# Performance work log

Hardware: AMD Instinct MI355X
Metric: run time of the kernel (lower is better)

## Reference

```python
import jax, jax.numpy as jnp
import numpy as np

N_HEAD = 16

def setup_inputs() -> dict:
    key = jax.random.key(0)
    k0, k1, k2, k3 = jax.random.split(key, 4)
    S, E, H, T = 2048, 1024, N_HEAD, 4096
    d = E // H
    return {
        "x": jax.random.normal(k0, (S, E), jnp.float32),
        "past": jax.random.normal(k1, (2, H, T, d), jnp.float32),  # stacked [pk, pv]
        "W1": jax.random.normal(k2, (E, 3 * E), jnp.float32) * 0.02,  # c_attn (Conv1D k=1 == linear)
        "b1": jnp.zeros((3 * E,), jnp.float32),
        "W2": jax.random.normal(k3, (E, E), jnp.float32) * 0.02,  # c_proj
        "b2": jnp.zeros((E,), jnp.float32),
        "past_length": 2048,
    }


def reference(x, past, W1, b1, W2, b2, past_length):
    H = N_HEAD
    S, E = x.shape
    d = E // H

    c = x @ W1 + b1  # [S, 3E]
    q, k, v = jnp.split(c, 3, axis=1)

    def split_heads(t):  # [S, E] -> [H, S, d]
        return jnp.transpose(t.reshape(S, H, d), (1, 0, 2))

    q, k, v = split_heads(q), split_heads(k), split_heads(v)

    pk, pv = past[0], past[1]  # [H, T, d]
    k = jax.lax.dynamic_update_slice_in_dim(pk, k, past_length, axis=1)
    v = jax.lax.dynamic_update_slice_in_dim(pv, v, past_length, axis=1)

    # attention scores [H, S, T]
    w = jnp.einsum('hid,hjd->hij', q, k) / np.sqrt(d)
    ns = k.shape[1]
    i = jnp.arange(S)[:, None]
    j = jnp.arange(ns)[None, :]
    b = (i >= j - past_length).astype(w.dtype)
    w = w * b - jnp.float32(1e10) * (1 - b)
    w = jax.nn.softmax(w, axis=-1)

    a = jnp.einsum('hij,hjd->hid', w, v)  # [H, S, d]
    # faithful to original: start index clamps to 0 since axis len == S
    a = jax.lax.dynamic_slice_in_dim(a, past_length, S, axis=1)
    a = jnp.transpose(a, (1, 0, 2)).reshape(S, E)  # merge heads

    out = a @ W2 + b2
    new_cache = jnp.stack([k, v], axis=0)
    return out, new_cache
```

## Files before the change

kernel.cpp:

```cpp
#include <hip/hip_runtime.h>
#include <hip/hip_bf16.h>
#include <stdint.h>


#define S_LEN 2048
#define E_DIM 1024
#define NHEAD 16
#define HDIM  64
#define T_LEN 4096
#define PASTL 2048

typedef __bf16 bf16x8 __attribute__((ext_vector_type(8)));
typedef __bf16 bf16x4 __attribute__((ext_vector_type(4)));
typedef float  f32x4  __attribute__((ext_vector_type(4)));

static __device__ __forceinline__ f32x4 mfma_bf16(bf16x8 a, bf16x8 b, f32x4 c) {
  return __builtin_amdgcn_mfma_f32_16x16x32_bf16(a, b, c, 0, 0, 0);
}

static __device__ __forceinline__ unsigned int f2bf(float f) {
  union { float f; unsigned int u; } v; v.f = f;
  unsigned int u = v.u;
  return (u + 0x7fffu + ((u >> 16) & 1u)) >> 16;
}

static __device__ __forceinline__ float bf2f(unsigned short u) {
  union { unsigned int u; float f; } v; v.u = (unsigned int)u << 16;
  return v.f;
}

#define GLOBAL_LOAD_LDS16(gptr, lptr)                                              \
  __builtin_amdgcn_global_load_lds(                                                \
      (const __attribute__((address_space(1))) unsigned int*)(gptr),               \
      (__attribute__((address_space(3))) unsigned int*)(lptr), 16, 0, 0)

__global__ __launch_bounds__(256) void prep_kernel(
    const float* __restrict__ past, const float* __restrict__ x,
    const float* __restrict__ W1, const float* __restrict__ W2,
    float* __restrict__ cache, unsigned short* __restrict__ kb,
    unsigned short* __restrict__ xb, unsigned short* __restrict__ w1t,
    unsigned short* __restrict__ w2t, unsigned short* __restrict__ vtb) {
  __shared__ float tile[64][65];
  const int bid = blockIdx.x;
  const int tid = threadIdx.x;
  const int tx = tid & 63, ty = tid >> 6;

  if (bid < 512) {
    const int h = bid >> 5;
    const int t0 = (bid & 31) * 64;
    const float* in = past + (size_t)(NHEAD + h) * T_LEN * HDIM;
    unsigned short* outp = vtb + (size_t)h * HDIM * T_LEN;
#pragma unroll
    for (int r = 0; r < 64; r += 4)
      tile[r + ty][tx] = in[(size_t)(t0 + r + ty) * HDIM + tx];
    __syncthreads();
#pragma unroll
    for (int r = 0; r < 64; r += 4)
      outp[(size_t)(r + ty) * T_LEN + t0 + tx] = f2bf(tile[tx][r + ty]);
  } else if (bid < 1536) {
    const float* in;
    unsigned short* outp;
    int rows, cols, c0, r0;
    if (bid < 1280) {
      int u = bid - 512;
      in = W1; outp = w1t; rows = 1024; cols = 3072;
      c0 = (u % 48) * 64; r0 = (u / 48) * 64;
    } else {
      int u = bid - 1280;
      in = W2; outp = w2t; rows = 1024; cols = 1024;
      c0 = (u & 15) * 64; r0 = (u >> 4) * 64;
    }
#pragma unroll
    for (int r = 0; r < 64; r += 4)
      tile[r + ty][tx] = in[(size_t)(r0 + r + ty) * cols + c0 + tx];
    __syncthreads();
#pragma unroll
    for (int r = 0; r < 64; r += 4)
      outp[(size_t)(c0 + r + ty) * rows + r0 + tx] = f2bf(tile[tx][r + ty]);
  } else {
    const int n4p = (2 * NHEAD * PASTL * HDIM) / 4;
    const int n4x = (S_LEN * E_DIM) / 4;
    for (int i = (bid - 1536) * 256 + tid; i < n4p + n4x; i += 2048 * 256) {
      if (i < n4p) {
        int e = i * 4;
        int d = e & 63;
        int t = (e >> 6) & (PASTL - 1);
        int hh = (e >> 17) & (NHEAD - 1);
        int kv = e >> 21;
        size_t full = (((size_t)kv * NHEAD + hh) * T_LEN + t) * HDIM + d;
        float4 v = *(const float4*)(past + full);
        *(float4*)(cache + full) = v;
        if (kv == 0) {
          ushort4 u;
          u.x = f2bf(v.x); u.y = f2bf(v.y); u.z = f2bf(v.z); u.w = f2bf(v.w);
          *(ushort4*)(kb + full) = u;
        }
      } else {
        int j = i - n4p;
        float4 v = ((const float4*)x)[j];
        ushort4 u;
        u.x = f2bf(v.x); u.y = f2bf(v.y); u.z = f2bf(v.z); u.w = f2bf(v.w);
        ((ushort4*)xb)[j] = u;
      }
    }
  }
}

template <int MODE>
__global__ __launch_bounds__(256) void gemm_bt_kernel(
    const unsigned short* __restrict__ A, const unsigned short* __restrict__ Bt,
    const float* __restrict__ bias, int K,
    float* __restrict__ out_f32, unsigned short* __restrict__ qb,
    float* __restrict__ cache_k, float* __restrict__ cache_v,
    unsigned short* __restrict__ kb, unsigned short* __restrict__ vtb) {
  __shared__ alignas(16) unsigned short As[64 * 64];
  __shared__ alignas(16) unsigned short Bs[128 * 64];
  const int NPX = (MODE == 0) ? 3 : 1;
  const int bid = blockIdx.x;
  const int xcd = bid & 7;
  const int loc = bid >> 3;
  const int n_idx = xcd * NPX + loc % NPX;
  const int m_idx = loc / NPX;
  const int m0 = m_idx * 64, n0 = n_idx * 128;

  const int tid = threadIdx.x;
  const int lane = tid & 63;
  const int w = tid >> 6;
  const int wm = w >> 1, wn = w & 1;
  const int lr = lane & 15;
  const int lg = lane >> 4;

  f32x4 acc[2][4];
#pragma unroll
  for (int i = 0; i < 2; ++i)
#pragma unroll
    for (int j = 0; j < 4; ++j) acc[i][j] = f32x4{0.f, 0.f, 0.f, 0.f};

  const int srow = tid >> 3;
  const int sseg = (tid & 7) ^ (srow & 7);
  const unsigned short* ga0 = A + (size_t)(m0 + srow) * K + sseg * 8;
  const unsigned short* gb0 = Bt + (size_t)(n0 + srow) * K + sseg * 8;

  for (int k0 = 0; k0 < K; k0 += 64) {
    GLOBAL_LOAD_LDS16(ga0 + k0, (char*)As + tid * 16);
    GLOBAL_LOAD_LDS16(ga0 + (size_t)32 * K + k0, (char*)As + 4096 + tid * 16);
#pragma unroll
    for (int j = 0; j < 4; ++j)
      GLOBAL_LOAD_LDS16(gb0 + (size_t)(32 * j) * K + k0,
                        (char*)Bs + j * 4096 + tid * 16);
    __syncthreads();
#pragma unroll
    for (int kk = 0; kk < 2; ++kk) {
      bf16x8 af[2], bfr[4];
#pragma unroll
      for (int mi = 0; mi < 2; ++mi) {
        int row = wm * 32 + mi * 16 + lr;
        int slot = (kk * 4 + lg) ^ (row & 7);
        af[mi] = *reinterpret_cast<const bf16x8*>((const char*)As + row * 128 + slot * 16);
      }
#pragma unroll
      for (int ni = 0; ni < 4; ++ni) {
        int row = wn * 64 + ni * 16 + lr;
        int slot = (kk * 4 + lg) ^ (row & 7);
        bfr[ni] = *reinterpret_cast<const bf16x8*>((const char*)Bs + row * 128 + slot * 16);
      }
#pragma unroll
      for (int mi = 0; mi < 2; ++mi)
#pragma unroll
        for (int ni = 0; ni < 4; ++ni)
          acc[mi][ni] = mfma_bf16(af[mi], bfr[ni], acc[mi][ni]);
    }
    __syncthreads();
  }

#pragma unroll
  for (int ni = 0; ni < 4; ++ni) {
    int n = n0 + wn * 64 + ni * 16 + lr;
    float bv = bias[n];
#pragma unroll
    for (int mi = 0; mi < 2; ++mi) {
      int mbase = m0 + wm * 32 + mi * 16 + lg * 4;
      float v4[4];
#pragma unroll
      for (int r = 0; r < 4; ++r) v4[r] = acc[mi][ni][r] + bv;
      if (MODE == 0) {
        if (n < E_DIM) {
#pragma unroll
          for (int r = 0; r < 4; ++r)
            qb[(size_t)(mbase + r) * E_DIM + n] = f2bf(v4[r] * 0.18033688f);
        } else if (n < 2 * E_DIM) {
          int e = n - E_DIM;
          size_t base = ((size_t)(e >> 6) * T_LEN + (PASTL + mbase)) * HDIM + (e & 63);
#pragma unroll
          for (int r = 0; r < 4; ++r) {
            cache_k[base + (size_t)r * HDIM] = v4[r];
            kb[base + (size_t)r * HDIM] = f2bf(v4[r]);
          }
        } else {
          int e = n - 2 * E_DIM;
          int hh = e >> 6, d = e & 63;
          size_t base = ((size_t)hh * T_LEN + (PASTL + mbase)) * HDIM + d;
#pragma unroll
          for (int r = 0; r < 4; ++r) cache_v[base + (size_t)r * HDIM] = v4[r];
          ushort4 u;
          u.x = f2bf(v4[0]); u.y = f2bf(v4[1]);
          u.z = f2bf(v4[2]); u.w = f2bf(v4[3]);
          *(ushort4*)(vtb + ((size_t)hh * HDIM + d) * T_LEN + PASTL + mbase) = u;
        }
      } else {
#pragma unroll
        for (int r = 0; r < 4; ++r)
          out_f32[(size_t)(mbase + r) * E_DIM + n] = v4[r];
      }
    }
  }
}

__global__ __launch_bounds__(256) void attn_kernel(
    const unsigned short* __restrict__ qb, const unsigned short* __restrict__ kb,
    const unsigned short* __restrict__ vt,
    unsigned short* __restrict__ o_part, float* __restrict__ l_part) {
  __shared__ alignas(16) unsigned short Ks[2][64 * 64];
  __shared__ alignas(16) unsigned short Vs[2][64 * 64];
  __shared__ alignas(16) __bf16 p_lds[4][32][72];
  const int fid = blockIdx.x;
  const int h = (fid & 7) + ((fid >= 448) ? 8 : 0);
  const int g = (fid >> 3) - ((fid >= 448) ? 56 : 0);
  int x, c;
  if (g < 24) { x = g / 3; c = g - 3 * x; }
  else { int g2 = g - 24; x = 8 + (g2 >> 2); c = g2 & 3; }

  const int tid = threadIdx.x;
  const int w = tid >> 6;
  const int lane = tid & 63;
  const int lr = lane & 15;
  const int lg = lane >> 4;
  const int qb0 = x * 128;
  const int q0 = qb0 + w * 32;

  const unsigned short* qr0 = qb + (size_t)(q0 + lr) * E_DIM + h * HDIM + lg * 8;
  const unsigned short* qr1 = qb + (size_t)(q0 + 16 + lr) * E_DIM + h * HDIM + lg * 8;
  const bf16x8 qf00 = *reinterpret_cast<const bf16x8*>(qr0);
  const bf16x8 qf01 = *reinterpret_cast<const bf16x8*>(qr0 + 32);
  const bf16x8 qf10 = *reinterpret_cast<const bf16x8*>(qr1);
  const bf16x8 qf11 = *reinterpret_cast<const bf16x8*>(qr1 + 32);

  const unsigned short* kh = kb + (size_t)h * T_LEN * HDIM;
  const unsigned short* vh = vt + (size_t)h * HDIM * T_LEN;

  const int srow = tid >> 3;
  const int sseg = (tid & 7) ^ (srow & 7);
  const unsigned short* ksrc = kh + (size_t)srow * HDIM + sseg * 8;
  const unsigned short* vsrc = vh + (size_t)srow * T_LEN + sseg * 8;

  f32x4 o[2][4];
  float lsum[2][2];
#pragma unroll
  for (int sb = 0; sb < 2; ++sb) {
    lsum[sb][0] = lsum[sb][1] = 0.f;
#pragma unroll
    for (int jd = 0; jd < 4; ++jd) o[sb][jd] = f32x4{0.f, 0.f, 0.f, 0.f};
  }

  const int jmaxq = q0 + PASTL;
  const int NTfull = 34 + 2 * x;
  const int tb = c * 16;
  const int te = (tb + 16 < NTfull) ? tb + 16 : NTfull;
  const int NT = te - tb;
  const int tbeg = tb * 64;

  auto stageK = [&](int b, int t0) {
    GLOBAL_LOAD_LDS16(ksrc + (size_t)t0 * HDIM, (char*)Ks[b] + tid * 16);
    GLOBAL_LOAD_LDS16(ksrc + (size_t)(t0 + 32) * HDIM, (char*)Ks[b] + 4096 + tid * 16);
  };
  auto stageV = [&](int b, int t0) {
    GLOBAL_LOAD_LDS16(vsrc + t0, (char*)Vs[b] + tid * 16);
    GLOBAL_LOAD_LDS16(vsrc + t0 + (size_t)32 * T_LEN, (char*)Vs[b] + 4096 + tid * 16);
  };

  stageK(0, tbeg);
  stageV(0, tbeg);
  int cur = 0;
  int t0 = tbeg;
  for (int i = 0; i < NT; ++i, t0 += 64) {
    const bool more = (i + 1 < NT);
    asm volatile("s_waitcnt vmcnt(2)" ::: "memory");
    __builtin_amdgcn_s_barrier();
    __builtin_amdgcn_sched_barrier(0);
    if (more) stageK(cur ^ 1, t0 + 64);

    bf16x8 kf[4][2];
#pragma unroll
    for (int j = 0; j < 4; ++j) {
      int row = j * 16 + lr;
      int s0 = lg ^ (row & 7), s1 = (4 + lg) ^ (row & 7);
      kf[j][0] = *reinterpret_cast<const bf16x8*>((const char*)Ks[cur] + row * 128 + s0 * 16);
      kf[j][1] = *reinterpret_cast<const bf16x8*>((const char*)Ks[cur] + row * 128 + s1 * 16);
    }

    f32x4 sc[2][4];
#pragma unroll
    for (int sb = 0; sb < 2; ++sb)
#pragma unroll
      for (int j = 0; j < 4; ++j) sc[sb][j] = f32x4{0.f, 0.f, 0.f, 0.f};
    __builtin_amdgcn_s_setprio(1);
#pragma unroll
    for (int j = 0; j < 4; ++j) {
      sc[0][j] = mfma_bf16(kf[j][0], qf00, sc[0][j]);
      sc[0][j] = mfma_bf16(kf[j][1], qf01, sc[0][j]);
      sc[1][j] = mfma_bf16(kf[j][0], qf10, sc[1][j]);
      sc[1][j] = mfma_bf16(kf[j][1], qf11, sc[1][j]);
    }
    __builtin_amdgcn_s_setprio(0);

    const bool partial = (t0 + 63 > jmaxq);
    const int thr = q0 + PASTL - t0 + lr;
    const int lg4 = lg * 4;
#pragma unroll
    for (int sb = 0; sb < 2; ++sb) {
#pragma unroll
      for (int j = 0; j < 4; ++j) {
        bf16x4 pk;
#pragma unroll
        for (int r = 0; r < 4; ++r) {
          float p = __builtin_amdgcn_exp2f(sc[sb][j][r]);
          if (partial && (j * 16 + lg4 + r > thr + sb * 16)) p = 0.f;
          lsum[sb][r >> 1] += p;
          pk[r] = (__bf16)p;
        }
        *reinterpret_cast<bf16x4*>(&p_lds[w][sb * 16 + lr][j * 16 + lg4]) = pk;
      }
    }
    bf16x8 pa[2][2];
#pragma unroll
    for (int sb = 0; sb < 2; ++sb) {
      pa[sb][0] = *reinterpret_cast<const bf16x8*>(&p_lds[w][sb * 16 + lr][lg * 8]);
      pa[sb][1] = *reinterpret_cast<const bf16x8*>(&p_lds[w][sb * 16 + lr][32 + lg * 8]);
    }

    if (more) {
      asm volatile("s_waitcnt vmcnt(2)" ::: "memory");
    } else {
      asm volatile("s_waitcnt vmcnt(0)" ::: "memory");
    }
    __builtin_amdgcn_s_barrier();
    __builtin_amdgcn_sched_barrier(0);
    if (more) stageV(cur ^ 1, t0 + 64);

    __builtin_amdgcn_s_setprio(1);
#pragma unroll
    for (int jd = 0; jd < 4; ++jd) {
      int row = jd * 16 + lr;
      int s0 = lg ^ (row & 7), s1 = (4 + lg) ^ (row & 7);
      bf16x8 vf0 = *reinterpret_cast<const bf16x8*>((const char*)Vs[cur] + row * 128 + s0 * 16);
      bf16x8 vf1 = *reinterpret_cast<const bf16x8*>((const char*)Vs[cur] + row * 128 + s1 * 16);
      o[0][jd] = mfma_bf16(pa[0][0], vf0, o[0][jd]);
      o[0][jd] = mfma_bf16(pa[0][1], vf1, o[0][jd]);
      o[1][jd] = mfma_bf16(pa[1][0], vf0, o[1][jd]);
      o[1][jd] = mfma_bf16(pa[1][1], vf1, o[1][jd]);
    }
    __builtin_amdgcn_s_setprio(0);
    cur ^= 1;
  }

  unsigned short* op = o_part + ((size_t)(c * NHEAD + h) * S_LEN) * HDIM;
  float* lp = l_part + (size_t)(c * NHEAD + h) * S_LEN;
#pragma unroll
  for (int sb = 0; sb < 2; ++sb) {
    float ls = lsum[sb][0] + lsum[sb][1];
    ls += __shfl_xor(ls, 16);
    ls += __shfl_xor(ls, 32);
    if (lg == 0) lp[q0 + sb * 16 + lr] = ls;
#pragma unroll
    for (int jd = 0; jd < 4; ++jd) {
#pragma unroll
      for (int r = 0; r < 4; ++r) {
        int row = q0 + sb * 16 + lg * 4 + r;
        op[(size_t)row * HDIM + jd * 16 + lr] = f2bf(o[sb][jd][r]);
      }
    }
  }
}

__global__ __launch_bounds__(256) void attn_merge_kernel(
    const unsigned short* __restrict__ o_part, const float* __restrict__ l_part,
    unsigned short* __restrict__ ab) {
  const int flat = blockIdx.x * 256 + threadIdx.x;
  const int d4 = flat & 15;
  const int row = (flat >> 4) & (S_LEN - 1);
  const int h = flat >> 15;
  const int nc = (row < 1024) ? 3 : 4;
  const size_t cstride_o = (size_t)NHEAD * S_LEN * HDIM;
  const size_t base_o = (((size_t)h * S_LEN) + row) * HDIM + d4 * 4;
  float acc[4] = {0.f, 0.f, 0.f, 0.f};
  float l = 0.f;
  for (int cc = 0; cc < nc; ++cc) {
    ushort4 u = *(const ushort4*)(o_part + cc * cstride_o + base_o);
    acc[0] += bf2f(u.x); acc[1] += bf2f(u.y);
    acc[2] += bf2f(u.z); acc[3] += bf2f(u.w);
    l += l_part[(size_t)cc * NHEAD * S_LEN + (size_t)h * S_LEN + row];
  }
  float inv = 1.f / l;
  ushort4 u;
  u.x = f2bf(acc[0] * inv);
  u.y = f2bf(acc[1] * inv);
  u.z = f2bf(acc[2] * inv);
  u.w = f2bf(acc[3] * inv);
  *(ushort4*)(ab + (size_t)row * E_DIM + h * HDIM + d4 * 4) = u;
}


extern "C" void kernel_launch(void* const* d_in, const int* in_sizes, int n_in,
                              void* d_out, int out_size, void* d_ws, size_t ws_size,
                              hipStream_t stream) {
  (void)in_sizes; (void)n_in; (void)out_size; (void)ws_size;
  const float* x    = (const float*)d_in[0];
  const float* past = (const float*)d_in[1];
  const float* W1   = (const float*)d_in[2];
  const float* b1   = (const float*)d_in[3];
  const float* W2   = (const float*)d_in[4];
  const float* b2   = (const float*)d_in[5];

  float* out = (float*)d_out;
  float* cache_k = out + (size_t)S_LEN * E_DIM;
  float* cache_v = cache_k + (size_t)NHEAD * T_LEN * HDIM;

  char* ws = (char*)d_ws;
  unsigned short* w2t = (unsigned short*)(ws);
  unsigned short* qb  = (unsigned short*)(ws + (size_t)(2u  << 20));
  unsigned short* kb  = (unsigned short*)(ws + (size_t)(6u  << 20));
  unsigned short* vtb = (unsigned short*)(ws + (size_t)(14u << 20));
  unsigned short* xb  = (unsigned short*)(ws + (size_t)(22u << 20));
  unsigned short* ab  = (unsigned short*)(ws + (size_t)(22u << 20));
  unsigned short* w1t = (unsigned short*)(ws + (size_t)(26u << 20));
  unsigned short* o_part = (unsigned short*)(ws + (size_t)(26u << 20));
  float* l_part = (float*)(ws + (size_t)(42u << 20));

  prep_kernel<<<3584, 256, 0, stream>>>(past, x, W1, W2, cache_k, kb, xb, w1t,
                                        w2t, vtb);
  gemm_bt_kernel<0><<<768, 256, 0, stream>>>(
      xb, w1t, b1, 1024, nullptr, qb, cache_k, cache_v, kb, vtb);
  attn_kernel<<<dim3(896), 256, 0, stream>>>(qb, kb, vtb, o_part, l_part);
  attn_merge_kernel<<<(NHEAD * S_LEN * 16) / 256, 256, 0, stream>>>(o_part, l_part, ab);
  gemm_bt_kernel<1><<<256, 256, 0, stream>>>(
      ab, w2t, b2, 1024, out, nullptr, nullptr, nullptr, nullptr, nullptr);
}
```

Baseline: 119.5 us.

## Rebalance attention split-K work with paired segments and fuse V-cache copy

The attention grid drops from 896 to 768 blocks. Short-tail chunks from different query tiles are paired so one block handles two segments in sequence, which evens out per-block work across the causal triangle. Separately, the past-V fp32 cache copy moves into the V transpose blocks, so the flat copy loop now only handles K. The risks are added per-segment setup inside the kernel and a different partition that the merge kernel must still match.

```diff
diff --git a/kernel.cpp b/kernel.cpp
--- a/kernel.cpp
+++ b/kernel.cpp
@@ -49,10 +49,14 @@
     const int h = bid >> 5;
     const int t0 = (bid & 31) * 64;
     const float* in = past + (size_t)(NHEAD + h) * T_LEN * HDIM;
+    float* outc = cache + (size_t)(NHEAD + h) * T_LEN * HDIM;
     unsigned short* outp = vtb + (size_t)h * HDIM * T_LEN;
 #pragma unroll
-    for (int r = 0; r < 64; r += 4)
-      tile[r + ty][tx] = in[(size_t)(t0 + r + ty) * HDIM + tx];
+    for (int r = 0; r < 64; r += 4) {
+      float v = in[(size_t)(t0 + r + ty) * HDIM + tx];
+      tile[r + ty][tx] = v;
+      outc[(size_t)(t0 + r + ty) * HDIM + tx] = v;
+    }
     __syncthreads();
 #pragma unroll
     for (int r = 0; r < 64; r += 4)
@@ -78,23 +82,20 @@
     for (int r = 0; r < 64; r += 4)
       outp[(size_t)(c0 + r + ty) * rows + r0 + tx] = f2bf(tile[tx][r + ty]);
   } else {
-    const int n4p = (2 * NHEAD * PASTL * HDIM) / 4;
+    const int n4p = (NHEAD * PASTL * HDIM) / 4;
     const int n4x = (S_LEN * E_DIM) / 4;
     for (int i = (bid - 1536) * 256 + tid; i < n4p + n4x; i += 2048 * 256) {
       if (i < n4p) {
         int e = i * 4;
         int d = e & 63;
         int t = (e >> 6) & (PASTL - 1);
-        int hh = (e >> 17) & (NHEAD - 1);
-        int kv = e >> 21;
-        size_t full = (((size_t)kv * NHEAD + hh) * T_LEN + t) * HDIM + d;
+        int hh = e >> 17;
+        size_t full = ((size_t)hh * T_LEN + t) * HDIM + d;
         float4 v = *(const float4*)(past + full);
         *(float4*)(cache + full) = v;
-        if (kv == 0) {
-          ushort4 u;
-          u.x = f2bf(v.x); u.y = f2bf(v.y); u.z = f2bf(v.z); u.w = f2bf(v.w);
-          *(ushort4*)(kb + full) = u;
-        }
+        ushort4 u;
+        u.x = f2bf(v.x); u.y = f2bf(v.y); u.z = f2bf(v.z); u.w = f2bf(v.w);
+        *(ushort4*)(kb + full) = u;
       } else {
         int j = i - n4p;
         float4 v = ((const float4*)x)[j];
@@ -224,26 +225,25 @@
   __shared__ alignas(16) unsigned short Vs[2][64 * 64];
   __shared__ alignas(16) __bf16 p_lds[4][32][72];
   const int fid = blockIdx.x;
-  const int h = (fid & 7) + ((fid >= 448) ? 8 : 0);
-  const int g = (fid >> 3) - ((fid >= 448) ? 56 : 0);
-  int x, c;
-  if (g < 24) { x = g / 3; c = g - 3 * x; }
-  else { int g2 = g - 24; x = 8 + (g2 >> 2); c = g2 & 3; }
+  const int h = (fid & 7) + ((fid >= 384) ? 8 : 0);
+  const int b = (fid >> 3) - ((fid >= 384) ? 48 : 0);
+
+  int nseg, x0s, c0s, x1s, c1s;
+  if (b < 16) {
+    nseg = 1; x0s = b >> 1; c0s = b & 1; x1s = 0; c1s = 0;
+  } else if (b < 40) {
+    int bb = b - 16;
+    nseg = 1; x0s = 8 + bb / 3; c0s = bb % 3; x1s = 0; c1s = 0;
+  } else {
+    int j = b - 40;
+    nseg = 2; x0s = j; c0s = 2; x1s = 15 - j; c1s = 3;
+  }
 
   const int tid = threadIdx.x;
   const int w = tid >> 6;
   const int lane = tid & 63;
   const int lr = lane & 15;
   const int lg = lane >> 4;
-  const int qb0 = x * 128;
-  const int q0 = qb0 + w * 32;
-
-  const unsigned short* qr0 = qb + (size_t)(q0 + lr) * E_DIM + h * HDIM + lg * 8;
-  const unsigned short* qr1 = qb + (size_t)(q0 + 16 + lr) * E_DIM + h * HDIM + lg * 8;
-  const bf16x8 qf00 = *reinterpret_cast<const bf16x8*>(qr0);
-  const bf16x8 qf01 = *reinterpret_cast<const bf16x8*>(qr0 + 32);
-  const bf16x8 qf10 = *reinterpret_cast<const bf16x8*>(qr1);
-  const bf16x8 qf11 = *reinterpret_cast<const bf16x8*>(qr1 + 32);
 
   const unsigned short* kh = kb + (size_t)h * T_LEN * HDIM;
   const unsigned short* vh = vt + (size_t)h * HDIM * T_LEN;
@@ -253,130 +253,144 @@
   const unsigned short* ksrc = kh + (size_t)srow * HDIM + sseg * 8;
   const unsigned short* vsrc = vh + (size_t)srow * T_LEN + sseg * 8;
 
-  f32x4 o[2][4];
-  float lsum[2][2];
-#pragma unroll
-  for (int sb = 0; sb < 2; ++sb) {
-    lsum[sb][0] = lsum[sb][1] = 0.f;
-#pragma unroll
-    for (int jd = 0; jd < 4; ++jd) o[sb][jd] = f32x4{0.f, 0.f, 0.f, 0.f};
-  }
-
-  const int jmaxq = q0 + PASTL;
-  const int NTfull = 34 + 2 * x;
-  const int tb = c * 16;
-  const int te = (tb + 16 < NTfull) ? tb + 16 : NTfull;
-  const int NT = te - tb;
-  const int tbeg = tb * 64;
-
-  auto stageK = [&](int b, int t0) {
-    GLOBAL_LOAD_LDS16(ksrc + (size_t)t0 * HDIM, (char*)Ks[b] + tid * 16);
-    GLOBAL_LOAD_LDS16(ksrc + (size_t)(t0 + 32) * HDIM, (char*)Ks[b] + 4096 + tid * 16);
+  auto stageK = [&](int bb, int t0) {
+    GLOBAL_LOAD_LDS16(ksrc + (size_t)t0 * HDIM, (char*)Ks[bb] + tid * 16);
+    GLOBAL_LOAD_LDS16(ksrc + (size_t)(t0 + 32) * HDIM, (char*)Ks[bb] + 4096 + tid * 16);
   };
-  auto stageV = [&](int b, int t0) {
-    GLOBAL_LOAD_LDS16(vsrc + t0, (char*)Vs[b] + tid * 16);
-    GLOBAL_LOAD_LDS16(vsrc + t0 + (size_t)32 * T_LEN, (char*)Vs[b] + 4096 + tid * 16);
+  auto stageV = [&](int bb, int t0) {
+    GLOBAL_LOAD_LDS16(vsrc + t0, (char*)Vs[bb] + tid * 16);
+    GLOBAL_LOAD_LDS16(vsrc + t0 + (size_t)32 * T_LEN, (char*)Vs[bb] + 4096 + tid * 16);
   };
 
-  stageK(0, tbeg);
-  stageV(0, tbeg);
   int cur = 0;
-  int t0 = tbeg;
-  for (int i = 0; i < NT; ++i, t0 += 64) {
-    const bool more = (i + 1 < NT);
-    asm volatile("s_waitcnt vmcnt(2)" ::: "memory");
-    __builtin_amdgcn_s_barrier();
-    __builtin_amdgcn_sched_barrier(0);
-    if (more) stageK(cur ^ 1, t0 + 64);
-
-    bf16x8 kf[4][2];
-#pragma unroll
-    for (int j = 0; j < 4; ++j) {
-      int row = j * 16 + lr;
-      int s0 = lg ^ (row & 7), s1 = (4 + lg) ^ (row & 7);
-      kf[j][0] = *reinterpret_cast<const bf16x8*>((const char*)Ks[cur] + row * 128 + s0 * 16);
-      kf[j][1] = *reinterpret_cast<const bf16x8*>((const char*)Ks[cur] + row * 128 + s1 * 16);
-    }
-
-    f32x4 sc[2][4];
-#pragma unroll
-    for (int sb = 0; sb < 2; ++sb)
-#pragma unroll
-      for (int j = 0; j < 4; ++j) sc[sb][j] = f32x4{0.f, 0.f, 0.f, 0.f};
-    __builtin_amdgcn_s_setprio(1);
-#pragma unroll
-    for (int j = 0; j < 4; ++j) {
-      sc[0][j] = mfma_bf16(kf[j][0], qf00, sc[0][j]);
-      sc[0][j] = mfma_bf16(kf[j][1], qf01, sc[0][j]);
-      sc[1][j] = mfma_bf16(kf[j][0], qf10, sc[1][j]);
-      sc[1][j] = mfma_bf16(kf[j][1], qf11, sc[1][j]);
-    }
-    __builtin_amdgcn_s_setprio(0);
-
-    const bool partial = (t0 + 63 > jmaxq);
-    const int thr = q0 + PASTL - t0 + lr;
-    const int lg4 = lg * 4;
+  for (int seg = 0; seg < nseg; ++seg) {
+    const int x = seg ? x1s : x0s;
+    const int c = seg ? c1s : c0s;
+    const int qb0 = x * 128;
+    const int q0 = qb0 + w * 32;
+
+    const unsigned short* qr0 = qb + (size_t)(q0 + lr) * E_DIM + h * HDIM + lg * 8;
+    const unsigned short* qr1 = qb + (size_t)(q0 + 16 + lr) * E_DIM + h * HDIM + lg * 8;
+    const bf16x8 qf00 = *reinterpret_cast<const bf16x8*>(qr0);
+    const bf16x8 qf01 = *reinterpret_cast<const bf16x8*>(qr0 + 32);
+    const bf16x8 qf10 = *reinterpret_cast<const bf16x8*>(qr1);
+    const bf16x8 qf11 = *reinterpret_cast<const bf16x8*>(qr1 + 32);
+
+    f32x4 o[2][4];
+    float lsum[2][2];
 #pragma unroll
     for (int sb = 0; sb < 2; ++sb) {
+      lsum[sb][0] = lsum[sb][1] = 0.f;
+#pragma unroll
+      for (int jd = 0; jd < 4; ++jd) o[sb][jd] = f32x4{0.f, 0.f, 0.f, 0.f};
+    }
+
+    const int jmaxq = q0 + PASTL;
+    const int NTfull = 34 + 2 * x;
+    const int tb = c * 16;
+    const int te = (tb + 16 < NTfull) ? tb + 16 : NTfull;
+    const int NT = te - tb;
+    const int tbeg = tb * 64;
+
+    stageK(cur, tbeg);
+    stageV(cur, tbeg);
+    int t0 = tbeg;
+    for (int i = 0; i < NT; ++i, t0 += 64) {
+      const bool more = (i + 1 < NT);
+      asm volatile("s_waitcnt vmcnt(2)" ::: "memory");
+      __builtin_amdgcn_s_barrier();
+      __builtin_amdgcn_sched_barrier(0);
+      if (more) stageK(cur ^ 1, t0 + 64);
+
+      bf16x8 kf[4][2];
 #pragma unroll
       for (int j = 0; j < 4; ++j) {
-        bf16x4 pk;
+        int row = j * 16 + lr;
+        int s0 = lg ^ (row & 7), s1 = (4 + lg) ^ (row & 7);
+        kf[j][0] = *reinterpret_cast<const bf16x8*>((const char*)Ks[cur] + row * 128 + s0 * 16);
+        kf[j][1] = *reinterpret_cast<const bf16x8*>((const char*)Ks[cur] + row * 128 + s1 * 16);
+      }
+
+      f32x4 sc[2][4];
+#pragma unroll
+      for (int sb = 0; sb < 2; ++sb)
+#pragma unroll
+        for (int j = 0; j < 4; ++j) sc[sb][j] = f32x4{0.f, 0.f, 0.f, 0.f};
+      __builtin_amdgcn_s_setprio(1);
+#pragma unroll
+      for (int j = 0; j < 4; ++j) {
+        sc[0][j] = mfma_bf16(kf[j][0], qf00, sc[0][j]);
+        sc[0][j] = mfma_bf16(kf[j][1], qf01, sc[0][j]);
+        sc[1][j] = mfma_bf16(kf[j][0], qf10, sc[1][j]);
+        sc[1][j] = mfma_bf16(kf[j][1], qf11, sc[1][j]);
+      }
+      __builtin_amdgcn_s_setprio(0);
+
+      const bool partial = (t0 + 63 > jmaxq);
+      const int thr = q0 + PASTL - t0 + lr;
+      const int lg4 = lg * 4;
+#pragma unroll
+      for (int sb = 0; sb < 2; ++sb) {
+#pragma unroll
+        for (int j = 0; j < 4; ++j) {
+          bf16x4 pk;
+#pragma unroll
+          for (int r = 0; r < 4; ++r) {
+            float p = __builtin_amdgcn_exp2f(sc[sb][j][r]);
+            if (partial && (j * 16 + lg4 + r > thr + sb * 16)) p = 0.f;
+            lsum[sb][r >> 1] += p;
+            pk[r] = (__bf16)p;
+          }
+          *reinterpret_cast<bf16x4*>(&p_lds[w][sb * 16 + lr][j * 16 + lg4]) = pk;
+        }
+      }
+      bf16x8 pa[2][2];
+#pragma unroll
+      for (int sb = 0; sb < 2; ++sb) {
+        pa[sb][0] = *reinterpret_cast<const bf16x8*>(&p_lds[w][sb * 16 + lr][lg * 8]);
+        pa[sb][1] = *reinterpret_cast<const bf16x8*>(&p_lds[w][sb * 16 + lr][32 + lg * 8]);
+      }
+
+      if (more) {
+        asm volatile("s_waitcnt vmcnt(2)" ::: "memory");
+      } else {
+        asm volatile("s_waitcnt vmcnt(0)" ::: "memory");
+      }
+      __builtin_amdgcn_s_barrier();
+      __builtin_amdgcn_sched_barrier(0);
+      if (more) stageV(cur ^ 1, t0 + 64);
+
+      __builtin_amdgcn_s_setprio(1);
+#pragma unroll
+      for (int jd = 0; jd < 4; ++jd) {
+        int row = jd * 16 + lr;
+        int s0 = lg ^ (row & 7), s1 = (4 + lg) ^ (row & 7);
+        bf16x8 vf0 = *reinterpret_cast<const bf16x8*>((const char*)Vs[cur] + row * 128 + s0 * 16);
+        bf16x8 vf1 = *reinterpret_cast<const bf16x8*>((const char*)Vs[cur] + row * 128 + s1 * 16);
+        o[0][jd] = mfma_bf16(pa[0][0], vf0, o[0][jd]);
+        o[0][jd] = mfma_bf16(pa[0][1], vf1, o[0][jd]);
+        o[1][jd] = mfma_bf16(pa[1][0], vf0, o[1][jd]);
+        o[1][jd] = mfma_bf16(pa[1][1], vf1, o[1][jd]);
+      }
+      __builtin_amdgcn_s_setprio(0);
+      cur ^= 1;
+    }
+
+    unsigned short* op = o_part + ((size_t)(c * NHEAD + h) * S_LEN) * HDIM;
+    float* lp = l_part + (size_t)(c * NHEAD + h) * S_LEN;
+#pragma unroll
+    for (int sb = 0; sb < 2; ++sb) {
+      float ls = lsum[sb][0] + lsum[sb][1];
+      ls += __shfl_xor(ls, 16);
+      ls += __shfl_xor(ls, 32);
+      if (lg == 0) lp[q0 + sb * 16 + lr] = ls;
+#pragma unroll
+      for (int jd = 0; jd < 4; ++jd) {
 #pragma unroll
         for (int r = 0; r < 4; ++r) {
-          float p = __builtin_amdgcn_exp2f(sc[sb][j][r]);
-          if (partial && (j * 16 + lg4 + r > thr + sb * 16)) p = 0.f;
-          lsum[sb][r >> 1] += p;
-          pk[r] = (__bf16)p;
+          int row = q0 + sb * 16 + lg * 4 + r;
+          op[(size_t)row * HDIM + jd * 16 + lr] = f2bf(o[sb][jd][r]);
         }
-        *reinterpret_cast<bf16x4*>(&p_lds[w][sb * 16 + lr][j * 16 + lg4]) = pk;
-      }
-    }
-    bf16x8 pa[2][2];
-#pragma unroll
-    for (int sb = 0; sb < 2; ++sb) {
-      pa[sb][0] = *reinterpret_cast<const bf16x8*>(&p_lds[w][sb * 16 + lr][lg * 8]);
-      pa[sb][1] = *reinterpret_cast<const bf16x8*>(&p_lds[w][sb * 16 + lr][32 + lg * 8]);
-    }
-
-    if (more) {
-      asm volatile("s_waitcnt vmcnt(2)" ::: "memory");
-    } else {
-      asm volatile("s_waitcnt vmcnt(0)" ::: "memory");
-    }
-    __builtin_amdgcn_s_barrier();
-    __builtin_amdgcn_sched_barrier(0);
-    if (more) stageV(cur ^ 1, t0 + 64);
-
-    __builtin_amdgcn_s_setprio(1);
-#pragma unroll
-    for (int jd = 0; jd < 4; ++jd) {
-      int row = jd * 16 + lr;
-      int s0 = lg ^ (row & 7), s1 = (4 + lg) ^ (row & 7);
-      bf16x8 vf0 = *reinterpret_cast<const bf16x8*>((const char*)Vs[cur] + row * 128 + s0 * 16);
-      bf16x8 vf1 = *reinterpret_cast<const bf16x8*>((const char*)Vs[cur] + row * 128 + s1 * 16);
-      o[0][jd] = mfma_bf16(pa[0][0], vf0, o[0][jd]);
-      o[0][jd] = mfma_bf16(pa[0][1], vf1, o[0][jd]);
-      o[1][jd] = mfma_bf16(pa[1][0], vf0, o[1][jd]);
-      o[1][jd] = mfma_bf16(pa[1][1], vf1, o[1][jd]);
-    }
-    __builtin_amdgcn_s_setprio(0);
-    cur ^= 1;
-  }
-
-  unsigned short* op = o_part + ((size_t)(c * NHEAD + h) * S_LEN) * HDIM;
-  float* lp = l_part + (size_t)(c * NHEAD + h) * S_LEN;
-#pragma unroll
-  for (int sb = 0; sb < 2; ++sb) {
-    float ls = lsum[sb][0] + lsum[sb][1];
-    ls += __shfl_xor(ls, 16);
-    ls += __shfl_xor(ls, 32);
-    if (lg == 0) lp[q0 + sb * 16 + lr] = ls;
-#pragma unroll
-    for (int jd = 0; jd < 4; ++jd) {
-#pragma unroll
-      for (int r = 0; r < 4; ++r) {
-        int row = q0 + sb * 16 + lg * 4 + r;
-        op[(size_t)row * HDIM + jd * 16 + lr] = f2bf(o[sb][jd][r]);
       }
     }
   }
@@ -440,7 +454,7 @@
                                         w2t, vtb);
   gemm_bt_kernel<0><<<768, 256, 0, stream>>>(
       xb, w1t, b1, 1024, nullptr, qb, cache_k, cache_v, kb, vtb);
-  attn_kernel<<<dim3(896), 256, 0, stream>>>(qb, kb, vtb, o_part, l_part);
+  attn_kernel<<<dim3(768), 256, 0, stream>>>(qb, kb, vtb, o_part, l_part);
   attn_merge_kernel<<<(NHEAD * S_LEN * 16) / 256, 256, 0, stream>>>(o_part, l_part, ab);
   gemm_bt_kernel<1><<<256, 256, 0, stream>>>(
       ab, w2t, b2, 1024, out, nullptr, nullptr, nullptr, nullptr, nullptr);
```

New measurement: 127.1 us. +6.4%, slower.
